# Kernel tuning notes

Hardware: AMD Instinct MI355X
Metric: run time of the kernel (lower is better)

## Reference

```python
import jax, jax.numpy as jnp
import numpy as np

B, L, D, H, N = 8, 2048, 128, 4, 2
DK = D // H          # 32
DFF = 2 * D          # 256 (dff = d * 2 in source)


def _init_proj(key, shape):
    # matches torch init: uniform in [-s, s], s = sqrt(6/(fan_in+fan_out)) of last two dims
    s = np.sqrt(6.0 / (shape[-1] + shape[-2]))
    return jax.random.uniform(key, shape, jnp.float32, -s, s)


def setup_inputs() -> dict:
    key = jax.random.key(0)
    ks = jax.random.split(key, 8)
    x = jax.random.normal(ks[0], (B, L, D), jnp.float32)
    mask = jnp.ones((B, L), jnp.float32)
    Wq = _init_proj(ks[1], (N, H, D, DK))
    Wk = _init_proj(ks[2], (N, H, D, DK))
    Wv = _init_proj(ks[3], (N, H, D, DK))
    Wo = _init_proj(ks[4], (N, H * DK, D))
    W1 = _init_proj(ks[5], (N, D, DFF))
    b1 = jnp.zeros((N, 1, 1, DFF), jnp.float32)
    W2 = _init_proj(ks[6], (N, DFF, D))
    b2 = jnp.zeros((N, 1, 1, D), jnp.float32)
    return {"x": x, "mask": mask, "Wq": Wq, "Wk": Wk, "Wv": Wv,
            "Wo": Wo, "W1": W1, "b1": b1, "W2": W2, "b2": b2}


def reference(x, mask, Wq, Wk, Wv, Wo, W1, b1, W2, b2):
    # Eval-mode forward (no attention dropout-mask trick, no FFN dropout).
    neg = jnp.finfo(x.dtype).min
    m2 = mask[:, :, None] * mask[:, None, :]              # [B, L, L]
    add_mask = (1.0 - m2)[:, None, :, :] * neg            # [B, 1, L, L]
    bsz, max_len, _ = x.shape
    for i in range(N):  # small fixed layer loop
        q = jnp.einsum('bld,hde->bhle', x, Wq[i])         # [B,H,L,DK]
        k = jnp.einsum('bld,hde->bhle', x, Wk[i])
        v = jnp.einsum('bld,hde->bhle', x, Wv[i])
        A = jnp.einsum('bhqe,bhke->bhqk', q, k) + add_mask  # note: no 1/sqrt(dk), as in source
        A = jax.nn.softmax(A, axis=-1)                    # [B,H,L,L]
        o = jnp.einsum('bhqk,bhke->bqhe', A, v)           # [B,L,H,DK]
        o = o.reshape(bsz, max_len, H * DK) @ Wo[i]       # [B,L,D]
        x = (o + x) / 2
        f = jax.nn.gelu(x @ W1[i] + b1[i], approximate=False)  # torch F.gelu is exact erf
        f = f @ W2[i] + b2[i]
        x = (f + x) / 2
    return x
```

## Files before the change

### kernel.cpp

```cpp
#include <hip/hip_runtime.h>
#include <math.h>

#define BB 8
#define LL 2048
#define DD 128
#define HH 4
#define DKK 32
#define DFFF 256

#define NEGMIN (-3.402823466e38f)
#define LOG2E 1.44269504088896f

typedef _Float16 f16;
typedef _Float16 f16x4 __attribute__((ext_vector_type(4)));
typedef _Float16 f16x8 __attribute__((ext_vector_type(8)));
typedef __fp16 h16x2 __attribute__((ext_vector_type(2)));
typedef float f32x4 __attribute__((ext_vector_type(4)));

union PKU { h16x2 h2[2]; f16x4 v; };

__global__ __launch_bounds__(256) void xcvt_kernel(const float* __restrict__ x,
                                                   f16* __restrict__ xh) {
  const int i = (blockIdx.x * 256 + threadIdx.x) * 8;
  float4 v0 = *(const float4*)(x + i);
  float4 v1 = *(const float4*)(x + i + 4);
  f16x8 h;
  h[0] = (f16)v0.x; h[1] = (f16)v0.y; h[2] = (f16)v0.z; h[3] = (f16)v0.w;
  h[4] = (f16)v1.x; h[5] = (f16)v1.y; h[6] = (f16)v1.z; h[7] = (f16)v1.w;
  *(f16x8*)(xh + i) = h;
}

__global__ __launch_bounds__(256) void wconv_kernel(
    const float* __restrict__ Wq, const float* __restrict__ Wk,
    const float* __restrict__ Wv, const float* __restrict__ Wo,
    const float* __restrict__ W1, const float* __restrict__ W2,
    f16* __restrict__ wt) {
  const int idx = blockIdx.x * 256 + threadIdx.x;
  const int i = idx >> 17;
  const int r = idx & 131071;
  float val;
  if (r < 49152) {
    const int sel = r / 16384;
    const int rr = r & 16383;
    const int n = rr >> 7, k = rr & 127;
    const float* W = (sel == 0) ? Wq : (sel == 1) ? Wk : Wv;
    val = W[((size_t)(i * 4 + (n >> 5)) * 128 + k) * 32 + (n & 31)];
  } else if (r < 65536) {
    const int r2 = r - 49152;
    const int n = r2 >> 7, k = r2 & 127;
    val = Wo[i * 16384 + k * 128 + n];
  } else if (r < 98304) {
    const int r2 = r - 65536;
    const int n = r2 >> 7, k = r2 & 127;
    val = W1[i * 32768 + k * 256 + n];
  } else {
    const int r2 = r - 98304;
    const int n = r2 >> 8, k = r2 & 255;
    val = W2[i * 32768 + k * 128 + n];
  }
  wt[idx] = (f16)val;
}

__global__ __launch_bounds__(256) void qkv_kernel(
    const f16* __restrict__ xh, const f16* __restrict__ wqkvT,
    f16* __restrict__ qh, f16* __restrict__ kh, f16* __restrict__ vth) {
  const int t = threadIdx.x;
  const int wave = t >> 6, lane = t & 63;
  const int g = lane >> 4, c = lane & 15;
  const int r0g = blockIdx.x * 64 + wave * 16;
  const int b4 = (r0g >> 11) * 4;
  const int l0 = r0g & 2047;

  f16x8 a[4];
#pragma unroll
  for (int kt = 0; kt < 4; ++kt)
    a[kt] = *(const f16x8*)(xh + (size_t)(r0g + c) * 128 + kt * 32 + g * 8);

#pragma unroll
  for (int sel = 0; sel < 2; ++sel) {
    const f16* wT = wqkvT + sel * 16384;
    f16* out = (sel == 0) ? qh : kh;
#pragma unroll
    for (int nt = 0; nt < 8; ++nt) {
      f32x4 acc = {0.f, 0.f, 0.f, 0.f};
#pragma unroll
      for (int kt = 0; kt < 4; ++kt) {
        f16x8 bfrag = *(const f16x8*)(wT + (nt * 16 + c) * 128 + kt * 32 + g * 8);
        acc = __builtin_amdgcn_mfma_f32_16x16x32_f16(a[kt], bfrag, acc, 0, 0, 0);
      }
      const int h = nt >> 1, e = (nt & 1) * 16 + c;
#pragma unroll
      for (int r = 0; r < 4; ++r)
        out[((size_t)(b4 + h) * LL + l0 + 4 * g + r) * DKK + e] = (f16)acc[r];
    }
  }
  {
    const f16* wT = wqkvT + 2 * 16384;
#pragma unroll
    for (int nt = 0; nt < 8; ++nt) {
      f32x4 acc = {0.f, 0.f, 0.f, 0.f};
#pragma unroll
      for (int kt = 0; kt < 4; ++kt) {
        f16x8 afrag = *(const f16x8*)(wT + (nt * 16 + c) * 128 + kt * 32 + g * 8);
        acc = __builtin_amdgcn_mfma_f32_16x16x32_f16(afrag, a[kt], acc, 0, 0, 0);
      }
#pragma unroll
      for (int r = 0; r < 4; ++r) {
        const int eg = nt * 16 + 4 * g + r;
        vth[((size_t)(b4 + (eg >> 5)) * DKK + (eg & 31)) * LL + l0 + c] =
            (f16)acc[r];
      }
    }
  }
}

__global__ __launch_bounds__(256) void attn_kernel(
    const f16* __restrict__ qh, const f16* __restrict__ kh,
    const f16* __restrict__ vth, const float* __restrict__ mask,
    f16* __restrict__ o) {
  __shared__ f16 Ks[2][64][40];
  __shared__ f16 Vt[2][32][72];
  __shared__ float mks[2][64];
  __shared__ int mkflag[2];
  const int t = threadIdx.x;
  const int wave = t >> 6, lane = t & 63;
  const int g = lane >> 4, c = lane & 15;

  const int flat = blockIdx.y * 16 + blockIdx.x;
  const int xcd = flat & 7, slot = flat >> 3;
  const int bh = xcd * 4 + (slot >> 4);
  const int qb = slot & 15;
  const int b = bh >> 2;
  const int qw = qb * 128 + wave * 32;

  f16x8 qfrag[2];
  float mqv[2];
#pragma unroll
  for (int qt = 0; qt < 2; ++qt) {
    qfrag[qt] =
        *(const f16x8*)(qh + ((size_t)bh * LL + qw + qt * 16 + c) * DKK + g * 8);
    mqv[qt] = mask[b * LL + qw + qt * 16 + c];
  }
  const bool qflag = __all(mqv[0] == 1.f && mqv[1] == 1.f);

  f32x4 o4[2][2];
  float m[2], l[2];
#pragma unroll
  for (int qt = 0; qt < 2; ++qt) {
    m[qt] = -3.0e38f; l[qt] = 0.f;
#pragma unroll
    for (int dt = 0; dt < 2; ++dt)
#pragma unroll
      for (int r = 0; r < 4; ++r) o4[qt][dt][r] = 0.f;
  }

  const f16* kbase = kh + (size_t)bh * LL * DKK;
  const f16* vbase = vth + (size_t)bh * DKK * LL;
  const int krow = t >> 2, kch = t & 3;
  const int vd = t >> 3, vseg = t & 7;

  f16x8 kreg = *(const f16x8*)(kbase + (size_t)krow * DKK + kch * 8);
  f16x8 vreg = *(const f16x8*)(vbase + (size_t)vd * LL + vseg * 8);
  float mreg = (t < 64) ? mask[b * LL + t] : 1.f;
  *(f16x8*)&Ks[0][krow][kch * 8] = kreg;
  *(f16x8*)&Vt[0][vd][vseg * 8] = vreg;
  if (t < 64) mks[0][t] = mreg;
  if (wave == 0) {
    unsigned long long ok = __ballot(mreg == 1.f);
    if (lane == 0) mkflag[0] = (ok == ~0ull);
  }
  __syncthreads();

  for (int kt = 0; kt < LL / 64; ++kt) {
    const int cur = kt & 1;
    if (kt < LL / 64 - 1) {
      const int k0 = (kt + 1) * 64;
      kreg = *(const f16x8*)(kbase + (size_t)(k0 + krow) * DKK + kch * 8);
      vreg = *(const f16x8*)(vbase + (size_t)vd * LL + k0 + vseg * 8);
      mreg = (t < 64) ? mask[b * LL + k0 + t] : 1.f;
    }
    const bool nomask = qflag && mkflag[cur];

    f16x8 kb[4];
#pragma unroll
    for (int nt = 0; nt < 4; ++nt)
      kb[nt] = *(const f16x8*)&Ks[cur][nt * 16 + c][g * 8];
    f16x4 va[2][4];
#pragma unroll
    for (int dt = 0; dt < 2; ++dt)
#pragma unroll
      for (int nt = 0; nt < 4; ++nt)
        va[dt][nt] = *(const f16x4*)&Vt[cur][dt * 16 + c][nt * 16 + 4 * g];

    f32x4 st[2][4];
    __builtin_amdgcn_s_setprio(1);
#pragma unroll
    for (int qt = 0; qt < 2; ++qt)
#pragma unroll
      for (int nt = 0; nt < 4; ++nt) {
        f32x4 z = {0.f, 0.f, 0.f, 0.f};
        st[qt][nt] =
            __builtin_amdgcn_mfma_f32_16x16x32_f16(kb[nt], qfrag[qt], z, 0, 0, 0);
      }
    __builtin_amdgcn_s_setprio(0);

    if (!nomask) {
#pragma unroll
      for (int qt = 0; qt < 2; ++qt) {
        const float mq = mqv[qt];
#pragma unroll
        for (int nt = 0; nt < 4; ++nt) {
          float4 mk4 = *(const float4*)&mks[cur][nt * 16 + 4 * g];
          st[qt][nt][0] += (1.f - mq * mk4.x) * NEGMIN;
          st[qt][nt][1] += (1.f - mq * mk4.y) * NEGMIN;
          st[qt][nt][2] += (1.f - mq * mk4.z) * NEGMIN;
          st[qt][nt][3] += (1.f - mq * mk4.w) * NEGMIN;
        }
      }
    }

#pragma unroll
    for (int qt = 0; qt < 2; ++qt) {
      float vmax = fmaxf(fmaxf(st[qt][0][0], st[qt][0][1]),
                         fmaxf(st[qt][0][2], st[qt][0][3]));
#pragma unroll
      for (int nt = 1; nt < 4; ++nt)
        vmax = fmaxf(vmax, fmaxf(fmaxf(st[qt][nt][0], st[qt][nt][1]),
                                 fmaxf(st[qt][nt][2], st[qt][nt][3])));
      vmax = fmaxf(vmax, __shfl_xor(vmax, 16));
      vmax = fmaxf(vmax, __shfl_xor(vmax, 32));

      if (!__all(vmax - m[qt] <= 8.f)) {
        const float mn = fmaxf(m[qt], vmax);
        const float sc = __builtin_exp2f((m[qt] - mn) * LOG2E);
        l[qt] *= sc;
#pragma unroll
        for (int dt = 0; dt < 2; ++dt)
#pragma unroll
          for (int r = 0; r < 4; ++r) o4[qt][dt][r] *= sc;
        m[qt] = mn;
      }
      const float mn2 = m[qt] * LOG2E;

      float p[4][4];
      float psum = 0.f;
#pragma unroll
      for (int nt = 0; nt < 4; ++nt) {
#pragma unroll
        for (int r = 0; r < 4; ++r) {
          p[nt][r] = __builtin_exp2f(fmaf(st[qt][nt][r], LOG2E, -mn2));
          psum += p[nt][r];
        }
      }
      l[qt] += psum;

      __builtin_amdgcn_s_setprio(1);
#pragma unroll
      for (int nt = 0; nt < 4; ++nt) {
        PKU pk;
        pk.h2[0] = __builtin_amdgcn_cvt_pkrtz(p[nt][0], p[nt][1]);
        pk.h2[1] = __builtin_amdgcn_cvt_pkrtz(p[nt][2], p[nt][3]);
        o4[qt][0] = __builtin_amdgcn_mfma_f32_16x16x16f16(va[0][nt], pk.v,
                                                          o4[qt][0], 0, 0, 0);
        o4[qt][1] = __builtin_amdgcn_mfma_f32_16x16x16f16(va[1][nt], pk.v,
                                                          o4[qt][1], 0, 0, 0);
      }
      __builtin_amdgcn_s_setprio(0);
    }

    if (kt < LL / 64 - 1) {
      *(f16x8*)&Ks[1 - cur][krow][kch * 8] = kreg;
      *(f16x8*)&Vt[1 - cur][vd][vseg * 8] = vreg;
      if (t < 64) mks[1 - cur][t] = mreg;
      if (wave == 0) {
        unsigned long long ok = __ballot(mreg == 1.f);
        if (lane == 0) mkflag[1 - cur] = (ok == ~0ull);
      }
    }
    __syncthreads();
  }

  const int h = bh & 3;
#pragma unroll
  for (int qt = 0; qt < 2; ++qt) {
    float lt = l[qt];
    lt += __shfl_xor(lt, 16);
    lt += __shfl_xor(lt, 32);
    const float rdiv = 1.f / lt;
    f16* orow = o + ((size_t)b * LL + qw + qt * 16 + c) * DD + h * DKK;
#pragma unroll
    for (int dt = 0; dt < 2; ++dt) {
      f16x4 res;
      res[0] = (f16)(o4[qt][dt][0] * rdiv);
      res[1] = (f16)(o4[qt][dt][1] * rdiv);
      res[2] = (f16)(o4[qt][dt][2] * rdiv);
      res[3] = (f16)(o4[qt][dt][3] * rdiv);
      *(f16x4*)(orow + dt * 16 + g * 4) = res;
    }
  }
}

__global__ __launch_bounds__(256) void mlp_kernel(
    const f16* __restrict__ o, const float* __restrict__ x,
    const f16* __restrict__ WoT, const f16* __restrict__ W1T,
    const f16* __restrict__ W2T, const float* __restrict__ b1,
    const float* __restrict__ b2, float* __restrict__ xout,
    const f16* __restrict__ wqkvT_next,
    f16* __restrict__ qh, f16* __restrict__ kh, f16* __restrict__ vth) {
  __shared__ f16 Xm[64][136];
  __shared__ f16 Fs[64][264];
  const int t = threadIdx.x;
  const int wave = t >> 6, lane = t & 63;
  const int g = lane >> 4, c = lane & 15;
  const int mrow = wave * 16;
  const long r0 = (long)blockIdx.x * 64;

  f16x8 a1[4];
#pragma unroll
  for (int kt = 0; kt < 4; ++kt)
    a1[kt] = *(const f16x8*)(o + (r0 + mrow + c) * 128 + kt * 32 + g * 8);

  f32x4 xmreg[8];
#pragma unroll
  for (int nt = 0; nt < 8; ++nt) {
    f32x4 acc = {0.f, 0.f, 0.f, 0.f};
#pragma unroll
    for (int kt = 0; kt < 4; ++kt) {
      f16x8 bfrag = *(const f16x8*)(WoT + (nt * 16 + c) * 128 + kt * 32 + g * 8);
      acc = __builtin_amdgcn_mfma_f32_16x16x32_f16(a1[kt], bfrag, acc, 0, 0, 0);
    }
#pragma unroll
    for (int r = 0; r < 4; ++r) {
      const float xv = x[(r0 + mrow + 4 * g + r) * 128 + nt * 16 + c];
      acc[r] = (acc[r] + xv) * 0.5f;
      Xm[mrow + 4 * g + r][nt * 16 + c] = (f16)acc[r];
    }
    xmreg[nt] = acc;
  }

  f16x8 a2[4];
#pragma unroll
  for (int kt = 0; kt < 4; ++kt)
    a2[kt] = *(const f16x8*)&Xm[mrow + c][kt * 32 + g * 8];
#pragma unroll
  for (int nt = 0; nt < 16; ++nt) {
    f32x4 acc = {0.f, 0.f, 0.f, 0.f};
#pragma unroll
    for (int kt = 0; kt < 4; ++kt) {
      f16x8 bfrag = *(const f16x8*)(W1T + (nt * 16 + c) * 128 + kt * 32 + g * 8);
      acc = __builtin_amdgcn_mfma_f32_16x16x32_f16(a2[kt], bfrag, acc, 0, 0, 0);
    }
    const float bj = b1[nt * 16 + c];
#pragma unroll
    for (int r = 0; r < 4; ++r) {
      const float val = acc[r] + bj;
      Fs[mrow + 4 * g + r][nt * 16 + c] =
          (f16)(0.5f * val * (1.f + erff(val * 0.70710678118654752f)));
    }
  }

  f16x8 a3[8];
#pragma unroll
  for (int kt = 0; kt < 8; ++kt)
    a3[kt] = *(const f16x8*)&Fs[mrow + c][kt * 32 + g * 8];
#pragma unroll
  for (int nt = 0; nt < 8; ++nt) {
    f32x4 acc = {0.f, 0.f, 0.f, 0.f};
#pragma unroll
    for (int kt = 0; kt < 8; ++kt) {
      f16x8 bfrag = *(const f16x8*)(W2T + (nt * 16 + c) * 256 + kt * 32 + g * 8);
      acc = __builtin_amdgcn_mfma_f32_16x16x32_f16(a3[kt], bfrag, acc, 0, 0, 0);
    }
    const float bj = b2[nt * 16 + c];
#pragma unroll
    for (int r = 0; r < 4; ++r) {
      const float val = (acc[r] + bj + xmreg[nt][r]) * 0.5f;
      xout[(r0 + mrow + 4 * g + r) * 128 + nt * 16 + c] = val;
      Xm[mrow + 4 * g + r][nt * 16 + c] = (f16)val;
    }
  }

  if (wqkvT_next) {
    const int r0g = (int)r0 + mrow;
    const int b4 = (r0g >> 11) * 4;
    const int l0 = r0g & 2047;
    f16x8 a[4];
#pragma unroll
    for (int kt = 0; kt < 4; ++kt)
      a[kt] = *(const f16x8*)&Xm[mrow + c][kt * 32 + g * 8];

#pragma unroll
    for (int sel = 0; sel < 2; ++sel) {
      const f16* wT = wqkvT_next + sel * 16384;
      f16* out = (sel == 0) ? qh : kh;
#pragma unroll
      for (int nt = 0; nt < 8; ++nt) {
        f32x4 acc = {0.f, 0.f, 0.f, 0.f};
#pragma unroll
        for (int kt = 0; kt < 4; ++kt) {
          f16x8 bfrag =
              *(const f16x8*)(wT + (nt * 16 + c) * 128 + kt * 32 + g * 8);
          acc = __builtin_amdgcn_mfma_f32_16x16x32_f16(a[kt], bfrag, acc, 0, 0, 0);
        }
        const int h = nt >> 1, e = (nt & 1) * 16 + c;
#pragma unroll
        for (int r = 0; r < 4; ++r)
          out[((size_t)(b4 + h) * LL + l0 + 4 * g + r) * DKK + e] = (f16)acc[r];
      }
    }
    {
      const f16* wT = wqkvT_next + 2 * 16384;
#pragma unroll
      for (int nt = 0; nt < 8; ++nt) {
        f32x4 acc = {0.f, 0.f, 0.f, 0.f};
#pragma unroll
        for (int kt = 0; kt < 4; ++kt) {
          f16x8 afrag =
              *(const f16x8*)(wT + (nt * 16 + c) * 128 + kt * 32 + g * 8);
          acc = __builtin_amdgcn_mfma_f32_16x16x32_f16(afrag, a[kt], acc, 0, 0, 0);
        }
#pragma unroll
        for (int r = 0; r < 4; ++r) {
          const int eg = nt * 16 + 4 * g + r;
          vth[((size_t)(b4 + (eg >> 5)) * DKK + (eg & 31)) * LL + l0 + c] =
              (f16)acc[r];
        }
      }
    }
  }
}

extern "C" void kernel_launch(void* const* d_in, const int* in_sizes, int n_in,
                              void* d_out, int out_size, void* d_ws,
                              size_t ws_size, hipStream_t stream) {
  const float* x    = (const float*)d_in[0];
  const float* mask = (const float*)d_in[1];
  const float* Wq   = (const float*)d_in[2];
  const float* Wk   = (const float*)d_in[3];
  const float* Wv   = (const float*)d_in[4];
  const float* Wo   = (const float*)d_in[5];
  const float* W1   = (const float*)d_in[6];
  const float* b1   = (const float*)d_in[7];
  const float* W2   = (const float*)d_in[8];
  const float* b2   = (const float*)d_in[9];

  const size_t SZ = (size_t)BB * LL * DD;
  char* p = (char*)d_ws;
  f16* qh   = (f16*)p;  p += SZ * sizeof(f16);
  f16* kh   = (f16*)p;  p += SZ * sizeof(f16);
  f16* vth  = (f16*)p;  p += SZ * sizeof(f16);
  f16* ob   = (f16*)p;  p += SZ * sizeof(f16);
  f16* xh0  = (f16*)p;  p += SZ * sizeof(f16);
  f16* wt   = (f16*)p;  p += (size_t)262144 * sizeof(f16);
  float* xA = (float*)p;

  wconv_kernel<<<1024, 256, 0, stream>>>(Wq, Wk, Wv, Wo, W1, W2, wt);
  xcvt_kernel<<<SZ / 8 / 256, 256, 0, stream>>>(x, xh0);

  for (int i = 0; i < 2; ++i) {
    const float* xin = (i == 0) ? x : xA;
    float* xout = (i == 1) ? (float*)d_out : xA;
    const f16* qkvT_i = wt + (size_t)i * 131072;
    const f16* WoT_i  = wt + (size_t)i * 131072 + 49152;
    const f16* W1T_i  = wt + (size_t)i * 131072 + 65536;
    const f16* W2T_i  = wt + (size_t)i * 131072 + 98304;
    const float* b1_i = b1 + (long)i * DFFF;
    const float* b2_i = b2 + (long)i * DD;
    const f16* qkvT_next = (i == 0) ? (wt + 131072) : nullptr;

    if (i == 0)
      qkv_kernel<<<(BB * LL) / 64, 256, 0, stream>>>(xh0, qkvT_i, qh, kh, vth);
    attn_kernel<<<dim3(LL / 128, BB * HH), 256, 0, stream>>>(qh, kh, vth, mask, ob);
    mlp_kernel<<<(BB * LL) / 64, 256, 0, stream>>>(ob, xin, WoT_i, W1T_i, W2T_i,
                                                   b1_i, b2_i, xout,
                                                   qkvT_next, qh, kh, vth);
  }
}
```

Measured before the change: 218.5 us.

## Halve attention query tile per wave and compute row sums with MFMA

Each wave now handles 16 query rows instead of 32, so blocks cover 64 queries and the grid doubles to 1024 blocks, giving more parallelism and lower register pressure. The softmax row sum is moved from scalar adds plus cross-lane shuffles onto an extra MFMA against a vector of ones, which also removes the shuffle reduction at the end. The cost is that K/V tiles are loaded from global memory and staged in LDS twice as often per query, and one more MFMA is issued per key sub-tile.

```diff
diff --git a/kernel.cpp b/kernel.cpp
--- a/kernel.cpp
+++ b/kernel.cpp
@@ -126,33 +126,24 @@
   const int wave = t >> 6, lane = t & 63;
   const int g = lane >> 4, c = lane & 15;
 
-  const int flat = blockIdx.y * 16 + blockIdx.x;
+  const int flat = blockIdx.y * 32 + blockIdx.x;
   const int xcd = flat & 7, slot = flat >> 3;
-  const int bh = xcd * 4 + (slot >> 4);
-  const int qb = slot & 15;
+  const int bh = xcd * 4 + (slot >> 5);
+  const int qb = slot & 31;
   const int b = bh >> 2;
-  const int qw = qb * 128 + wave * 32;
-
-  f16x8 qfrag[2];
-  float mqv[2];
-#pragma unroll
-  for (int qt = 0; qt < 2; ++qt) {
-    qfrag[qt] =
-        *(const f16x8*)(qh + ((size_t)bh * LL + qw + qt * 16 + c) * DKK + g * 8);
-    mqv[qt] = mask[b * LL + qw + qt * 16 + c];
-  }
-  const bool qflag = __all(mqv[0] == 1.f && mqv[1] == 1.f);
-
-  f32x4 o4[2][2];
-  float m[2], l[2];
-#pragma unroll
-  for (int qt = 0; qt < 2; ++qt) {
-    m[qt] = -3.0e38f; l[qt] = 0.f;
-#pragma unroll
-    for (int dt = 0; dt < 2; ++dt)
-#pragma unroll
-      for (int r = 0; r < 4; ++r) o4[qt][dt][r] = 0.f;
-  }
+  const int qw = qb * 64 + wave * 16;
+
+  const f16x8 qfrag =
+      *(const f16x8*)(qh + ((size_t)bh * LL + qw + c) * DKK + g * 8);
+  const float mqv = mask[b * LL + qw + c];
+  const bool qflag = __all(mqv == 1.f);
+
+  f32x4 o4[2], lacc;
+  float m = -3.0e38f;
+#pragma unroll
+  for (int r = 0; r < 4; ++r) { o4[0][r] = 0.f; o4[1][r] = 0.f; lacc[r] = 0.f; }
+  f16x4 ones;
+  ones[0] = (f16)1.f; ones[1] = (f16)1.f; ones[2] = (f16)1.f; ones[3] = (f16)1.f;
 
   const f16* kbase = kh + (size_t)bh * LL * DKK;
   const f16* vbase = vth + (size_t)bh * DKK * LL;
@@ -192,81 +183,67 @@
       for (int nt = 0; nt < 4; ++nt)
         va[dt][nt] = *(const f16x4*)&Vt[cur][dt * 16 + c][nt * 16 + 4 * g];
 
-    f32x4 st[2][4];
+    f32x4 st[4];
     __builtin_amdgcn_s_setprio(1);
 #pragma unroll
-    for (int qt = 0; qt < 2; ++qt)
+    for (int nt = 0; nt < 4; ++nt) {
+      f32x4 z = {0.f, 0.f, 0.f, 0.f};
+      st[nt] =
+          __builtin_amdgcn_mfma_f32_16x16x32_f16(kb[nt], qfrag, z, 0, 0, 0);
+    }
+    __builtin_amdgcn_s_setprio(0);
+
+    if (!nomask) {
 #pragma unroll
       for (int nt = 0; nt < 4; ++nt) {
-        f32x4 z = {0.f, 0.f, 0.f, 0.f};
-        st[qt][nt] =
-            __builtin_amdgcn_mfma_f32_16x16x32_f16(kb[nt], qfrag[qt], z, 0, 0, 0);
-      }
+        float4 mk4 = *(const float4*)&mks[cur][nt * 16 + 4 * g];
+        st[nt][0] += (1.f - mqv * mk4.x) * NEGMIN;
+        st[nt][1] += (1.f - mqv * mk4.y) * NEGMIN;
+        st[nt][2] += (1.f - mqv * mk4.z) * NEGMIN;
+        st[nt][3] += (1.f - mqv * mk4.w) * NEGMIN;
+      }
+    }
+
+    float vmax = fmaxf(fmaxf(st[0][0], st[0][1]), fmaxf(st[0][2], st[0][3]));
+#pragma unroll
+    for (int nt = 1; nt < 4; ++nt)
+      vmax = fmaxf(vmax, fmaxf(fmaxf(st[nt][0], st[nt][1]),
+                               fmaxf(st[nt][2], st[nt][3])));
+    vmax = fmaxf(vmax, __shfl_xor(vmax, 16));
+    vmax = fmaxf(vmax, __shfl_xor(vmax, 32));
+
+    if (!__all(vmax - m <= 8.f)) {
+      const float mn = fmaxf(m, vmax);
+      const float sc = __builtin_exp2f((m - mn) * LOG2E);
+#pragma unroll
+      for (int r = 0; r < 4; ++r) {
+        o4[0][r] *= sc; o4[1][r] *= sc; lacc[r] *= sc;
+      }
+      m = mn;
+    }
+    const float mn2 = m * LOG2E;
+
+    PKU pk[4];
+#pragma unroll
+    for (int nt = 0; nt < 4; ++nt) {
+      float p0 = __builtin_exp2f(fmaf(st[nt][0], LOG2E, -mn2));
+      float p1 = __builtin_exp2f(fmaf(st[nt][1], LOG2E, -mn2));
+      float p2 = __builtin_exp2f(fmaf(st[nt][2], LOG2E, -mn2));
+      float p3 = __builtin_exp2f(fmaf(st[nt][3], LOG2E, -mn2));
+      pk[nt].h2[0] = __builtin_amdgcn_cvt_pkrtz(p0, p1);
+      pk[nt].h2[1] = __builtin_amdgcn_cvt_pkrtz(p2, p3);
+    }
+    __builtin_amdgcn_s_setprio(1);
+#pragma unroll
+    for (int nt = 0; nt < 4; ++nt) {
+      o4[0] = __builtin_amdgcn_mfma_f32_16x16x16f16(va[0][nt], pk[nt].v,
+                                                    o4[0], 0, 0, 0);
+      o4[1] = __builtin_amdgcn_mfma_f32_16x16x16f16(va[1][nt], pk[nt].v,
+                                                    o4[1], 0, 0, 0);
+      lacc = __builtin_amdgcn_mfma_f32_16x16x16f16(ones, pk[nt].v,
+                                                   lacc, 0, 0, 0);
+    }
     __builtin_amdgcn_s_setprio(0);
-
-    if (!nomask) {
-#pragma unroll
-      for (int qt = 0; qt < 2; ++qt) {
-        const float mq = mqv[qt];
-#pragma unroll
-        for (int nt = 0; nt < 4; ++nt) {
-          float4 mk4 = *(const float4*)&mks[cur][nt * 16 + 4 * g];
-          st[qt][nt][0] += (1.f - mq * mk4.x) * NEGMIN;
-          st[qt][nt][1] += (1.f - mq * mk4.y) * NEGMIN;
-          st[qt][nt][2] += (1.f - mq * mk4.z) * NEGMIN;
-          st[qt][nt][3] += (1.f - mq * mk4.w) * NEGMIN;
-        }
-      }
-    }
-
-#pragma unroll
-    for (int qt = 0; qt < 2; ++qt) {
-      float vmax = fmaxf(fmaxf(st[qt][0][0], st[qt][0][1]),
-                         fmaxf(st[qt][0][2], st[qt][0][3]));
-#pragma unroll
-      for (int nt = 1; nt < 4; ++nt)
-        vmax = fmaxf(vmax, fmaxf(fmaxf(st[qt][nt][0], st[qt][nt][1]),
-                                 fmaxf(st[qt][nt][2], st[qt][nt][3])));
-      vmax = fmaxf(vmax, __shfl_xor(vmax, 16));
-      vmax = fmaxf(vmax, __shfl_xor(vmax, 32));
-
-      if (!__all(vmax - m[qt] <= 8.f)) {
-        const float mn = fmaxf(m[qt], vmax);
-        const float sc = __builtin_exp2f((m[qt] - mn) * LOG2E);
-        l[qt] *= sc;
-#pragma unroll
-        for (int dt = 0; dt < 2; ++dt)
-#pragma unroll
-          for (int r = 0; r < 4; ++r) o4[qt][dt][r] *= sc;
-        m[qt] = mn;
-      }
-      const float mn2 = m[qt] * LOG2E;
-
-      float p[4][4];
-      float psum = 0.f;
-#pragma unroll
-      for (int nt = 0; nt < 4; ++nt) {
-#pragma unroll
-        for (int r = 0; r < 4; ++r) {
-          p[nt][r] = __builtin_exp2f(fmaf(st[qt][nt][r], LOG2E, -mn2));
-          psum += p[nt][r];
-        }
-      }
-      l[qt] += psum;
-
-      __builtin_amdgcn_s_setprio(1);
-#pragma unroll
-      for (int nt = 0; nt < 4; ++nt) {
-        PKU pk;
-        pk.h2[0] = __builtin_amdgcn_cvt_pkrtz(p[nt][0], p[nt][1]);
-        pk.h2[1] = __builtin_amdgcn_cvt_pkrtz(p[nt][2], p[nt][3]);
-        o4[qt][0] = __builtin_amdgcn_mfma_f32_16x16x16f16(va[0][nt], pk.v,
-                                                          o4[qt][0], 0, 0, 0);
-        o4[qt][1] = __builtin_amdgcn_mfma_f32_16x16x16f16(va[1][nt], pk.v,
-                                                          o4[qt][1], 0, 0, 0);
-      }
-      __builtin_amdgcn_s_setprio(0);
-    }
 
     if (kt < LL / 64 - 1) {
       *(f16x8*)&Ks[1 - cur][krow][kch * 8] = kreg;
@@ -281,22 +258,16 @@
   }
 
   const int h = bh & 3;
-#pragma unroll
-  for (int qt = 0; qt < 2; ++qt) {
-    float lt = l[qt];
-    lt += __shfl_xor(lt, 16);
-    lt += __shfl_xor(lt, 32);
-    const float rdiv = 1.f / lt;
-    f16* orow = o + ((size_t)b * LL + qw + qt * 16 + c) * DD + h * DKK;
-#pragma unroll
-    for (int dt = 0; dt < 2; ++dt) {
-      f16x4 res;
-      res[0] = (f16)(o4[qt][dt][0] * rdiv);
-      res[1] = (f16)(o4[qt][dt][1] * rdiv);
-      res[2] = (f16)(o4[qt][dt][2] * rdiv);
-      res[3] = (f16)(o4[qt][dt][3] * rdiv);
-      *(f16x4*)(orow + dt * 16 + g * 4) = res;
-    }
+  const float rdiv = 1.f / lacc[0];
+  f16* orow = o + ((size_t)b * LL + qw + c) * DD + h * DKK;
+#pragma unroll
+  for (int dt = 0; dt < 2; ++dt) {
+    f16x4 res;
+    res[0] = (f16)(o4[dt][0] * rdiv);
+    res[1] = (f16)(o4[dt][1] * rdiv);
+    res[2] = (f16)(o4[dt][2] * rdiv);
+    res[3] = (f16)(o4[dt][3] * rdiv);
+    *(f16x4*)(orow + dt * 16 + g * 4) = res;
   }
 }
 
@@ -470,7 +441,7 @@
 
     if (i == 0)
       qkv_kernel<<<(BB * LL) / 64, 256, 0, stream>>>(xh0, qkvT_i, qh, kh, vth);
-    attn_kernel<<<dim3(LL / 128, BB * HH), 256, 0, stream>>>(qh, kh, vth, mask, ob);
+    attn_kernel<<<dim3(LL / 64, BB * HH), 256, 0, stream>>>(qh, kh, vth, mask, ob);
     mlp_kernel<<<(BB * LL) / 64, 256, 0, stream>>>(ob, xin, WoT_i, W1T_i, W2T_i,
                                                    b1_i, b2_i, xout,
                                                    qkvT_next, qh, kh, vth);
```

Result: slower. 226.7 us (+3.8%).

## Split attention KV range across two blocks and merge with combine kernel

Applied to the files above, without the earlier changes.

Attention now splits each query block's key/value range into two halves handled by separate blocks (1024 blocks instead of 512). Each block writes unnormalized fp32 partial outputs plus running max and sum, and a new combine kernel merges them into the fp16 output. A per-batch mask precheck kernel lets blocks skip per-tile mask loads and ballots when the whole batch row is unmasked. The goal is better occupancy across the GPU's compute units and less mask overhead. The cost is extra fp32 partial traffic and an additional kernel launch per layer.

```diff
diff --git a/kernel.cpp b/kernel.cpp
--- a/kernel.cpp
+++ b/kernel.cpp
@@ -28,6 +28,18 @@
   h[0] = (f16)v0.x; h[1] = (f16)v0.y; h[2] = (f16)v0.z; h[3] = (f16)v0.w;
   h[4] = (f16)v1.x; h[5] = (f16)v1.y; h[6] = (f16)v1.z; h[7] = (f16)v1.w;
   *(f16x8*)(xh + i) = h;
+}
+
+__global__ __launch_bounds__(256) void maskchk_kernel(
+    const float* __restrict__ mask, int* __restrict__ flags) {
+  __shared__ int wok[4];
+  const int b = blockIdx.x, t = threadIdx.x;
+  bool ok = true;
+  for (int i = t; i < LL; i += 256) ok &= (mask[b * LL + i] == 1.f);
+  const bool all_ok = __all(ok);
+  if ((t & 63) == 0) wok[t >> 6] = all_ok ? 1 : 0;
+  __syncthreads();
+  if (t == 0) flags[b] = wok[0] & wok[1] & wok[2] & wok[3];
 }
 
 __global__ __launch_bounds__(256) void wconv_kernel(
@@ -117,7 +129,8 @@
 __global__ __launch_bounds__(256) void attn_kernel(
     const f16* __restrict__ qh, const f16* __restrict__ kh,
     const f16* __restrict__ vth, const float* __restrict__ mask,
-    f16* __restrict__ o) {
+    const int* __restrict__ bflags, float* __restrict__ Opart,
+    float2* __restrict__ ml) {
   __shared__ f16 Ks[2][64][40];
   __shared__ f16 Vt[2][32][72];
   __shared__ float mks[2][64];
@@ -126,22 +139,28 @@
   const int wave = t >> 6, lane = t & 63;
   const int g = lane >> 4, c = lane & 15;
 
-  const int flat = blockIdx.y * 16 + blockIdx.x;
+  const int flat = blockIdx.x;
   const int xcd = flat & 7, slot = flat >> 3;
-  const int bh = xcd * 4 + (slot >> 4);
+  const int combo = xcd * 8 + (slot >> 4);
   const int qb = slot & 15;
+  const int bh = combo >> 1, z = combo & 1;
   const int b = bh >> 2;
   const int qw = qb * 128 + wave * 32;
+  const int kv0 = z * (LL / 2);
+  const bool nomask_b = (bflags[b] != 0);
 
   f16x8 qfrag[2];
-  float mqv[2];
-#pragma unroll
-  for (int qt = 0; qt < 2; ++qt) {
+  float mqv[2] = {1.f, 1.f};
+#pragma unroll
+  for (int qt = 0; qt < 2; ++qt)
     qfrag[qt] =
         *(const f16x8*)(qh + ((size_t)bh * LL + qw + qt * 16 + c) * DKK + g * 8);
-    mqv[qt] = mask[b * LL + qw + qt * 16 + c];
-  }
-  const bool qflag = __all(mqv[0] == 1.f && mqv[1] == 1.f);
+  bool qflag = true;
+  if (!nomask_b) {
+#pragma unroll
+    for (int qt = 0; qt < 2; ++qt) mqv[qt] = mask[b * LL + qw + qt * 16 + c];
+    qflag = __all(mqv[0] == 1.f && mqv[1] == 1.f);
+  }
 
   f32x4 o4[2][2];
   float m[2], l[2];
@@ -154,32 +173,36 @@
       for (int r = 0; r < 4; ++r) o4[qt][dt][r] = 0.f;
   }
 
-  const f16* kbase = kh + (size_t)bh * LL * DKK;
-  const f16* vbase = vth + (size_t)bh * DKK * LL;
+  const f16* kbase = kh + (size_t)bh * LL * DKK + (size_t)kv0 * DKK;
+  const f16* vbase = vth + (size_t)bh * DKK * LL + kv0;
   const int krow = t >> 2, kch = t & 3;
   const int vd = t >> 3, vseg = t & 7;
 
   f16x8 kreg = *(const f16x8*)(kbase + (size_t)krow * DKK + kch * 8);
   f16x8 vreg = *(const f16x8*)(vbase + (size_t)vd * LL + vseg * 8);
-  float mreg = (t < 64) ? mask[b * LL + t] : 1.f;
+  float mreg = 1.f;
   *(f16x8*)&Ks[0][krow][kch * 8] = kreg;
   *(f16x8*)&Vt[0][vd][vseg * 8] = vreg;
-  if (t < 64) mks[0][t] = mreg;
-  if (wave == 0) {
-    unsigned long long ok = __ballot(mreg == 1.f);
-    if (lane == 0) mkflag[0] = (ok == ~0ull);
+  if (!nomask_b) {
+    mreg = (t < 64) ? mask[b * LL + kv0 + t] : 1.f;
+    if (t < 64) mks[0][t] = mreg;
+    if (wave == 0) {
+      unsigned long long ok = __ballot(mreg == 1.f);
+      if (lane == 0) mkflag[0] = (ok == ~0ull);
+    }
   }
   __syncthreads();
 
-  for (int kt = 0; kt < LL / 64; ++kt) {
+  const int NTILES = (LL / 2) / 64;
+  for (int kt = 0; kt < NTILES; ++kt) {
     const int cur = kt & 1;
-    if (kt < LL / 64 - 1) {
+    if (kt < NTILES - 1) {
       const int k0 = (kt + 1) * 64;
       kreg = *(const f16x8*)(kbase + (size_t)(k0 + krow) * DKK + kch * 8);
       vreg = *(const f16x8*)(vbase + (size_t)vd * LL + k0 + vseg * 8);
-      mreg = (t < 64) ? mask[b * LL + k0 + t] : 1.f;
-    }
-    const bool nomask = qflag && mkflag[cur];
+      if (!nomask_b) mreg = (t < 64) ? mask[b * LL + kv0 + k0 + t] : 1.f;
+    }
+    const bool nomask = nomask_b || (qflag && mkflag[cur]);
 
     f16x8 kb[4];
 #pragma unroll
@@ -198,9 +221,9 @@
     for (int qt = 0; qt < 2; ++qt)
 #pragma unroll
       for (int nt = 0; nt < 4; ++nt) {
-        f32x4 z = {0.f, 0.f, 0.f, 0.f};
+        f32x4 zz = {0.f, 0.f, 0.f, 0.f};
         st[qt][nt] =
-            __builtin_amdgcn_mfma_f32_16x16x32_f16(kb[nt], qfrag[qt], z, 0, 0, 0);
+            __builtin_amdgcn_mfma_f32_16x16x32_f16(kb[nt], qfrag[qt], zz, 0, 0, 0);
       }
     __builtin_amdgcn_s_setprio(0);
 
@@ -268,36 +291,62 @@
       __builtin_amdgcn_s_setprio(0);
     }
 
-    if (kt < LL / 64 - 1) {
+    if (kt < NTILES - 1) {
       *(f16x8*)&Ks[1 - cur][krow][kch * 8] = kreg;
       *(f16x8*)&Vt[1 - cur][vd][vseg * 8] = vreg;
-      if (t < 64) mks[1 - cur][t] = mreg;
-      if (wave == 0) {
-        unsigned long long ok = __ballot(mreg == 1.f);
-        if (lane == 0) mkflag[1 - cur] = (ok == ~0ull);
+      if (!nomask_b) {
+        if (t < 64) mks[1 - cur][t] = mreg;
+        if (wave == 0) {
+          unsigned long long ok = __ballot(mreg == 1.f);
+          if (lane == 0) mkflag[1 - cur] = (ok == ~0ull);
+        }
       }
     }
     __syncthreads();
   }
 
-  const int h = bh & 3;
 #pragma unroll
   for (int qt = 0; qt < 2; ++qt) {
     float lt = l[qt];
     lt += __shfl_xor(lt, 16);
     lt += __shfl_xor(lt, 32);
-    const float rdiv = 1.f / lt;
-    f16* orow = o + ((size_t)b * LL + qw + qt * 16 + c) * DD + h * DKK;
+    const int qrow = qw + qt * 16 + c;
+    if (g == 0) ml[(size_t)z * 65536 + (size_t)bh * LL + qrow] =
+        make_float2(m[qt], lt);
+    float* obase = Opart + (size_t)z * 2097152 +
+                   ((size_t)bh * LL + qrow) * 32;
 #pragma unroll
     for (int dt = 0; dt < 2; ++dt) {
-      f16x4 res;
-      res[0] = (f16)(o4[qt][dt][0] * rdiv);
-      res[1] = (f16)(o4[qt][dt][1] * rdiv);
-      res[2] = (f16)(o4[qt][dt][2] * rdiv);
-      res[3] = (f16)(o4[qt][dt][3] * rdiv);
-      *(f16x4*)(orow + dt * 16 + g * 4) = res;
-    }
-  }
+      float4 res;
+      res.x = o4[qt][dt][0]; res.y = o4[qt][dt][1];
+      res.z = o4[qt][dt][2]; res.w = o4[qt][dt][3];
+      *(float4*)(obase + dt * 16 + g * 4) = res;
+    }
+  }
+}
+
+__global__ __launch_bounds__(256) void comb_kernel(
+    const float* __restrict__ Opart, const float2* __restrict__ ml,
+    f16* __restrict__ o) {
+  const int idx = blockIdx.x * 256 + threadIdx.x;
+  const int j4 = idx & 7;
+  const int rq = idx >> 3;
+  const int bh = rq >> 11, q = rq & 2047;
+  const int b = bh >> 2, h = bh & 3;
+  const float2 e0 = ml[rq];
+  const float2 e1 = ml[65536 + rq];
+  const float M = fmaxf(e0.x, e1.x);
+  const float w0 = __builtin_exp2f((e0.x - M) * LOG2E);
+  const float w1 = __builtin_exp2f((e1.x - M) * LOG2E);
+  const float rdiv = 1.f / (w0 * e0.y + w1 * e1.y);
+  const float4 a0 = *(const float4*)(Opart + (size_t)rq * 32 + j4 * 4);
+  const float4 a1 = *(const float4*)(Opart + 2097152 + (size_t)rq * 32 + j4 * 4);
+  f16x4 res;
+  res[0] = (f16)((w0 * a0.x + w1 * a1.x) * rdiv);
+  res[1] = (f16)((w0 * a0.y + w1 * a1.y) * rdiv);
+  res[2] = (f16)((w0 * a0.z + w1 * a1.z) * rdiv);
+  res[3] = (f16)((w0 * a0.w + w1 * a1.w) * rdiv);
+  *(f16x4*)(o + ((size_t)b * LL + q) * DD + h * DKK + j4 * 4) = res;
 }
 
 __global__ __launch_bounds__(256) void mlp_kernel(
@@ -452,10 +501,14 @@
   f16* ob   = (f16*)p;  p += SZ * sizeof(f16);
   f16* xh0  = (f16*)p;  p += SZ * sizeof(f16);
   f16* wt   = (f16*)p;  p += (size_t)262144 * sizeof(f16);
+  int* bflags = (int*)p; p += 256;
+  float2* ml = (float2*)p; p += (size_t)2 * 65536 * sizeof(float2);
+  float* Opart = (float*)p; p += (size_t)2 * 2097152 * sizeof(float);
   float* xA = (float*)p;
 
   wconv_kernel<<<1024, 256, 0, stream>>>(Wq, Wk, Wv, Wo, W1, W2, wt);
   xcvt_kernel<<<SZ / 8 / 256, 256, 0, stream>>>(x, xh0);
+  maskchk_kernel<<<BB, 256, 0, stream>>>(mask, bflags);
 
   for (int i = 0; i < 2; ++i) {
     const float* xin = (i == 0) ? x : xA;
@@ -470,7 +523,8 @@
 
     if (i == 0)
       qkv_kernel<<<(BB * LL) / 64, 256, 0, stream>>>(xh0, qkvT_i, qh, kh, vth);
-    attn_kernel<<<dim3(LL / 128, BB * HH), 256, 0, stream>>>(qh, kh, vth, mask, ob);
+    attn_kernel<<<1024, 256, 0, stream>>>(qh, kh, vth, mask, bflags, Opart, ml);
+    comb_kernel<<<2048, 256, 0, stream>>>(Opart, ml, ob);
     mlp_kernel<<<(BB * LL) / 64, 256, 0, stream>>>(ob, xin, WoT_i, W1T_i, W2T_i,
                                                    b1_i, b2_i, xout,
                                                    qkvT_next, qh, kh, vth);
```

Measured after the change: 229.5 us. 5.0% more time.

## Load K/V directly to registers with ping-pong prefetch, drop LDS and barriers

Applied to the files above, without the earlier changes.

The attention kernel no longer stages K and V tiles through shared memory behind per-tile __syncthreads. Each wave now loads its MFMA fragments straight from global memory into two register buffers that alternate, so the next tile's loads overlap the current tile's compute. A new small kernel checks once per batch row whether the mask is all ones, replacing the per-tile mask ballot, and masked rows read the key mask directly from global. The trade-off is that the four waves each fetch the same K/V data through the cache instead of sharing it, and register pressure goes up.

```diff
diff --git a/kernel.cpp b/kernel.cpp
--- a/kernel.cpp
+++ b/kernel.cpp
@@ -28,6 +28,18 @@
   h[0] = (f16)v0.x; h[1] = (f16)v0.y; h[2] = (f16)v0.z; h[3] = (f16)v0.w;
   h[4] = (f16)v1.x; h[5] = (f16)v1.y; h[6] = (f16)v1.z; h[7] = (f16)v1.w;
   *(f16x8*)(xh + i) = h;
+}
+
+__global__ __launch_bounds__(256) void maskchk_kernel(
+    const float* __restrict__ mask, int* __restrict__ flags) {
+  __shared__ int wok[4];
+  const int b = blockIdx.x, t = threadIdx.x;
+  bool ok = true;
+  for (int i = t; i < LL; i += 256) ok &= (mask[b * LL + i] == 1.f);
+  const bool all_ok = __all(ok);
+  if ((t & 63) == 0) wok[t >> 6] = all_ok ? 1 : 0;
+  __syncthreads();
+  if (t == 0) flags[b] = wok[0] & wok[1] & wok[2] & wok[3];
 }
 
 __global__ __launch_bounds__(256) void wconv_kernel(
@@ -117,31 +129,29 @@
 __global__ __launch_bounds__(256) void attn_kernel(
     const f16* __restrict__ qh, const f16* __restrict__ kh,
     const f16* __restrict__ vth, const float* __restrict__ mask,
-    f16* __restrict__ o) {
-  __shared__ f16 Ks[2][64][40];
-  __shared__ f16 Vt[2][32][72];
-  __shared__ float mks[2][64];
-  __shared__ int mkflag[2];
+    const int* __restrict__ bflags, f16* __restrict__ o) {
   const int t = threadIdx.x;
   const int wave = t >> 6, lane = t & 63;
   const int g = lane >> 4, c = lane & 15;
 
-  const int flat = blockIdx.y * 16 + blockIdx.x;
+  const int flat = blockIdx.x;
   const int xcd = flat & 7, slot = flat >> 3;
   const int bh = xcd * 4 + (slot >> 4);
   const int qb = slot & 15;
   const int b = bh >> 2;
   const int qw = qb * 128 + wave * 32;
+  const bool nomask_b = (bflags[b] != 0);
 
   f16x8 qfrag[2];
-  float mqv[2];
-#pragma unroll
-  for (int qt = 0; qt < 2; ++qt) {
+  float mqv[2] = {1.f, 1.f};
+#pragma unroll
+  for (int qt = 0; qt < 2; ++qt)
     qfrag[qt] =
         *(const f16x8*)(qh + ((size_t)bh * LL + qw + qt * 16 + c) * DKK + g * 8);
-    mqv[qt] = mask[b * LL + qw + qt * 16 + c];
-  }
-  const bool qflag = __all(mqv[0] == 1.f && mqv[1] == 1.f);
+  if (!nomask_b) {
+#pragma unroll
+    for (int qt = 0; qt < 2; ++qt) mqv[qt] = mask[b * LL + qw + qt * 16 + c];
+  }
 
   f32x4 o4[2][2];
   float m[2], l[2];
@@ -154,44 +164,36 @@
       for (int r = 0; r < 4; ++r) o4[qt][dt][r] = 0.f;
   }
 
-  const f16* kbase = kh + (size_t)bh * LL * DKK;
-  const f16* vbase = vth + (size_t)bh * DKK * LL;
-  const int krow = t >> 2, kch = t & 3;
-  const int vd = t >> 3, vseg = t & 7;
-
-  f16x8 kreg = *(const f16x8*)(kbase + (size_t)krow * DKK + kch * 8);
-  f16x8 vreg = *(const f16x8*)(vbase + (size_t)vd * LL + vseg * 8);
-  float mreg = (t < 64) ? mask[b * LL + t] : 1.f;
-  *(f16x8*)&Ks[0][krow][kch * 8] = kreg;
-  *(f16x8*)&Vt[0][vd][vseg * 8] = vreg;
-  if (t < 64) mks[0][t] = mreg;
-  if (wave == 0) {
-    unsigned long long ok = __ballot(mreg == 1.f);
-    if (lane == 0) mkflag[0] = (ok == ~0ull);
-  }
-  __syncthreads();
-
-  for (int kt = 0; kt < LL / 64; ++kt) {
-    const int cur = kt & 1;
-    if (kt < LL / 64 - 1) {
-      const int k0 = (kt + 1) * 64;
-      kreg = *(const f16x8*)(kbase + (size_t)(k0 + krow) * DKK + kch * 8);
-      vreg = *(const f16x8*)(vbase + (size_t)vd * LL + k0 + vseg * 8);
-      mreg = (t < 64) ? mask[b * LL + k0 + t] : 1.f;
-    }
-    const bool nomask = qflag && mkflag[cur];
-
-    f16x8 kb[4];
-#pragma unroll
-    for (int nt = 0; nt < 4; ++nt)
-      kb[nt] = *(const f16x8*)&Ks[cur][nt * 16 + c][g * 8];
-    f16x4 va[2][4];
-#pragma unroll
-    for (int dt = 0; dt < 2; ++dt)
-#pragma unroll
-      for (int nt = 0; nt < 4; ++nt)
-        va[dt][nt] = *(const f16x4*)&Vt[cur][dt * 16 + c][nt * 16 + 4 * g];
-
+  const f16* kp = kh + (size_t)bh * LL * DKK + (size_t)c * DKK + g * 8;
+  const f16* vp0 = vth + (size_t)bh * DKK * LL + (size_t)c * LL + 4 * g;
+  const f16* vp1 = vp0 + (size_t)16 * LL;
+
+#define LOADK(DST, KT)                                       \
+  {                                                          \
+    const f16* _p = kp + (size_t)(KT) * 64 * DKK;            \
+    DST[0] = *(const f16x8*)(_p);                            \
+    DST[1] = *(const f16x8*)(_p + 16 * DKK);                 \
+    DST[2] = *(const f16x8*)(_p + 32 * DKK);                 \
+    DST[3] = *(const f16x8*)(_p + 48 * DKK);                 \
+  }
+#define LOADV(DST, KT)                                       \
+  {                                                          \
+    const f16* _p0 = vp0 + (KT) * 64;                        \
+    const f16* _p1 = vp1 + (KT) * 64;                        \
+    DST[0] = *(const f16x4*)(_p0);                           \
+    DST[1] = *(const f16x4*)(_p0 + 16);                      \
+    DST[2] = *(const f16x4*)(_p0 + 32);                      \
+    DST[3] = *(const f16x4*)(_p0 + 48);                      \
+    DST[4] = *(const f16x4*)(_p1);                           \
+    DST[5] = *(const f16x4*)(_p1 + 16);                      \
+    DST[6] = *(const f16x4*)(_p1 + 32);                      \
+    DST[7] = *(const f16x4*)(_p1 + 48);                      \
+  }
+
+  f16x8 kbA[4], kbB[4];
+  f16x4 vaA[8], vaB[8];
+
+  auto compute = [&](const f16x8 (&kb)[4], const f16x4 (&va)[8], int k0) {
     f32x4 st[2][4];
     __builtin_amdgcn_s_setprio(1);
 #pragma unroll
@@ -204,13 +206,13 @@
       }
     __builtin_amdgcn_s_setprio(0);
 
-    if (!nomask) {
+    if (!nomask_b) {
 #pragma unroll
       for (int qt = 0; qt < 2; ++qt) {
         const float mq = mqv[qt];
 #pragma unroll
         for (int nt = 0; nt < 4; ++nt) {
-          float4 mk4 = *(const float4*)&mks[cur][nt * 16 + 4 * g];
+          float4 mk4 = *(const float4*)(mask + b * LL + k0 + nt * 16 + 4 * g);
           st[qt][nt][0] += (1.f - mq * mk4.x) * NEGMIN;
           st[qt][nt][1] += (1.f - mq * mk4.y) * NEGMIN;
           st[qt][nt][2] += (1.f - mq * mk4.z) * NEGMIN;
@@ -260,25 +262,29 @@
         PKU pk;
         pk.h2[0] = __builtin_amdgcn_cvt_pkrtz(p[nt][0], p[nt][1]);
         pk.h2[1] = __builtin_amdgcn_cvt_pkrtz(p[nt][2], p[nt][3]);
-        o4[qt][0] = __builtin_amdgcn_mfma_f32_16x16x16f16(va[0][nt], pk.v,
+        o4[qt][0] = __builtin_amdgcn_mfma_f32_16x16x16f16(va[nt], pk.v,
                                                           o4[qt][0], 0, 0, 0);
-        o4[qt][1] = __builtin_amdgcn_mfma_f32_16x16x16f16(va[1][nt], pk.v,
+        o4[qt][1] = __builtin_amdgcn_mfma_f32_16x16x16f16(va[4 + nt], pk.v,
                                                           o4[qt][1], 0, 0, 0);
       }
       __builtin_amdgcn_s_setprio(0);
     }
-
-    if (kt < LL / 64 - 1) {
-      *(f16x8*)&Ks[1 - cur][krow][kch * 8] = kreg;
-      *(f16x8*)&Vt[1 - cur][vd][vseg * 8] = vreg;
-      if (t < 64) mks[1 - cur][t] = mreg;
-      if (wave == 0) {
-        unsigned long long ok = __ballot(mreg == 1.f);
-        if (lane == 0) mkflag[1 - cur] = (ok == ~0ull);
-      }
-    }
-    __syncthreads();
-  }
+  };
+
+  LOADK(kbA, 0);
+  LOADV(vaA, 0);
+  for (int kt = 0; kt < 32; kt += 2) {
+    LOADK(kbB, kt + 1);
+    LOADV(vaB, kt + 1);
+    compute(kbA, vaA, kt * 64);
+    if (kt + 2 < 32) {
+      LOADK(kbA, kt + 2);
+      LOADV(vaA, kt + 2);
+    }
+    compute(kbB, vaB, (kt + 1) * 64);
+  }
+#undef LOADK
+#undef LOADV
 
   const int h = bh & 3;
 #pragma unroll
@@ -452,10 +458,12 @@
   f16* ob   = (f16*)p;  p += SZ * sizeof(f16);
   f16* xh0  = (f16*)p;  p += SZ * sizeof(f16);
   f16* wt   = (f16*)p;  p += (size_t)262144 * sizeof(f16);
+  int* bflags = (int*)p; p += 256;
   float* xA = (float*)p;
 
   wconv_kernel<<<1024, 256, 0, stream>>>(Wq, Wk, Wv, Wo, W1, W2, wt);
   xcvt_kernel<<<SZ / 8 / 256, 256, 0, stream>>>(x, xh0);
+  maskchk_kernel<<<BB, 256, 0, stream>>>(mask, bflags);
 
   for (int i = 0; i < 2; ++i) {
     const float* xin = (i == 0) ? x : xA;
@@ -470,7 +478,7 @@
 
     if (i == 0)
       qkv_kernel<<<(BB * LL) / 64, 256, 0, stream>>>(xh0, qkvT_i, qh, kh, vth);
-    attn_kernel<<<dim3(LL / 128, BB * HH), 256, 0, stream>>>(qh, kh, vth, mask, ob);
+    attn_kernel<<<512, 256, 0, stream>>>(qh, kh, vth, mask, bflags, ob);
     mlp_kernel<<<(BB * LL) / 64, 256, 0, stream>>>(ob, xin, WoT_i, W1T_i, W2T_i,
                                                    b1_i, b2_i, xout,
                                                    qkvT_next, qh, kh, vth);
```

After: 249.9 us. 1.14x slower.
